# Kernel optimization log

Measured on AMD Instinct MI355X. Metric: run time of the kernel, lower is better.

## Reference

```python
import jax, jax.numpy as jnp
import numpy as np

B, S, F_IN = 2048, 256, 3
COND = 4
EMBED = 4
HID = 64
NUM_CODES = 256
BETA = 0.25


def _linear_params(key, fan_in, fan_out):
    k1, k2 = jax.random.split(key)
    lim = 1.0 / np.sqrt(fan_in)
    w = jax.random.uniform(k1, (fan_in, fan_out), jnp.float32, -lim, lim)
    b = jax.random.uniform(k2, (fan_out,), jnp.float32, -lim, lim)
    return w, b


def setup_inputs() -> dict:
    key = jax.random.key(0)
    ks = jax.random.split(key, 10)
    x = jax.random.normal(ks[0], (B, S, F_IN), jnp.float32)
    mask = jnp.ones((B, S), jnp.float32)
    x_conditional = jax.random.normal(ks[1], (B, COND), jnp.float32)
    enc_w1, enc_b1 = _linear_params(ks[2], F_IN + COND, HID)
    enc_w2, enc_b2 = _linear_params(ks[3], HID, HID)
    enc_w3, enc_b3 = _linear_params(ks[4], HID, EMBED)
    codebook = jax.random.normal(ks[5], (NUM_CODES, EMBED), jnp.float32)
    dec_w1, dec_b1 = _linear_params(ks[6], EMBED + COND, HID)
    dec_w2, dec_b2 = _linear_params(ks[7], HID, HID)
    dec_w3, dec_b3 = _linear_params(ks[8], HID, F_IN)
    return dict(x=x, mask=mask, x_conditional=x_conditional,
                enc_w1=enc_w1, enc_b1=enc_b1, enc_w2=enc_w2, enc_b2=enc_b2,
                enc_w3=enc_w3, enc_b3=enc_b3, codebook=codebook,
                dec_w1=dec_w1, dec_b1=dec_b1, dec_w2=dec_w2, dec_b2=dec_b2,
                dec_w3=dec_w3, dec_b3=dec_b3)


def _mlp(x, w1, b1, w2, b2, w3, b3):
    h = jax.nn.relu(x @ w1 + b1)
    h = jax.nn.relu(h @ w2 + b2)
    return h @ w3 + b3


def _vq(z, codebook):
    # z: [B, S, E]; nearest-codebook assignment via expanded squared L2
    zf = z.reshape(-1, z.shape[-1])                       # [N, E]
    d = (jnp.sum(zf * zf, axis=-1, keepdims=True)
         - 2.0 * zf @ codebook.T
         + jnp.sum(codebook * codebook, axis=-1))         # [N, num_codes]
    idx = jnp.argmin(d, axis=-1)                          # [N]
    z_q = codebook[idx].reshape(z.shape)                  # [B, S, E]
    # VQ losses (codebook + beta * commitment)
    loss = (jnp.mean((jax.lax.stop_gradient(z) - z_q) ** 2)
            + BETA * jnp.mean((z - jax.lax.stop_gradient(z_q)) ** 2))
    # straight-through estimator
    z_q_st = z + jax.lax.stop_gradient(z_q - z)
    return z_q_st, loss, idx.reshape(z.shape[:-1])


def reference(x, mask, x_conditional,
              enc_w1, enc_b1, enc_w2, enc_b2, enc_w3, enc_b3,
              codebook,
              dec_w1, dec_b1, dec_w2, dec_b2, dec_w3, dec_b3):
    cond = jnp.broadcast_to(x_conditional[:, None, :], (B, S, COND))
    xin = jnp.concatenate([x, cond], axis=-1) * mask[..., None]
    z = _mlp(xin, enc_w1, enc_b1, enc_w2, enc_b2, enc_w3, enc_b3)
    z_q, vq_loss, idx = _vq(z, codebook)
    zdec = jnp.concatenate([z_q, cond], axis=-1) * mask[..., None]
    x_reco = _mlp(zdec, dec_w1, dec_b1, dec_w2, dec_b2, dec_w3, dec_b3)
    return x_reco, vq_loss, idx
```

## Files before the change

kernel.cpp:

```cpp
#include <hip/hip_runtime.h>
#include <hip/hip_bf16.h>

#define BB   2048
#define SS   256
#define NTOK (BB*SS)
#define FIN  3
#define CND  4
#define EMB  4
#define HID  64
#define NC   256
#define TPB  256

#define OF_EW1 0
#define OF_EB1 448
#define OF_EW2 512
#define OF_EB2 4608
#define OF_EW3 4672
#define OF_EB3 4928
#define OF_CB  4944
#define OF_CC  5968
#define OF_DW1 6224
#define OF_DB1 6736
#define OF_DW2 6800
#define OF_DB2 10896
#define OF_DW3 10960
#define OF_DB3 11152
#define SMEM_F 11168

__global__ __launch_bounds__(TPB, 2) void vqvae_fused(
        const float* __restrict__ x, const float* __restrict__ mask,
        const float* __restrict__ cond,
        const float* __restrict__ ew1, const float* __restrict__ eb1,
        const float* __restrict__ ew2, const float* __restrict__ eb2,
        const float* __restrict__ ew3, const float* __restrict__ eb3,
        const float* __restrict__ cb,
        const float* __restrict__ dw1, const float* __restrict__ db1,
        const float* __restrict__ dw2, const float* __restrict__ db2,
        const float* __restrict__ dw3, const float* __restrict__ db3,
        float* __restrict__ out, float* __restrict__ loss_ws) {
    __shared__ float smem[SMEM_F];
    const int tid = threadIdx.x;

    for (int i = tid; i < (FIN+CND)*HID; i += TPB) smem[OF_EW1+i] = ew1[i];
    for (int i = tid; i < HID;           i += TPB) smem[OF_EB1+i] = eb1[i];
    for (int i = tid; i < HID*HID;       i += TPB) smem[OF_EW2+i] = ew2[i];
    for (int i = tid; i < HID;           i += TPB) smem[OF_EB2+i] = eb2[i];
    for (int i = tid; i < HID*EMB;       i += TPB) smem[OF_EW3+i] = ew3[i];
    for (int i = tid; i < EMB;           i += TPB) smem[OF_EB3+i] = eb3[i];
    for (int i = tid; i < NC*EMB;        i += TPB) smem[OF_CB +i] = cb[i];
    for (int i = tid; i < (EMB+CND)*HID; i += TPB) smem[OF_DW1+i] = dw1[i];
    for (int i = tid; i < HID;           i += TPB) smem[OF_DB1+i] = db1[i];
    for (int i = tid; i < HID*HID;       i += TPB) smem[OF_DW2+i] = dw2[i];
    for (int i = tid; i < HID;           i += TPB) smem[OF_DB2+i] = db2[i];
    for (int i = tid; i < HID*FIN;       i += TPB) smem[OF_DW3+i] = dw3[i];
    for (int i = tid; i < FIN;           i += TPB) smem[OF_DB3+i] = db3[i];
    {
        float c0 = cb[tid*EMB+0], c1 = cb[tid*EMB+1];
        float c2 = cb[tid*EMB+2], c3 = cb[tid*EMB+3];
        smem[OF_CC+tid] = ((c0*c0 + c1*c1) + c2*c2) + c3*c3;
    }
    __syncthreads();

    const int n0 = blockIdx.x * (2*TPB) + tid;
    const int n1 = n0 + TPB;
    const float m0 = mask[n0];
    const float m1 = mask[n1];
    const int bu0 = n0 >> 8;
    const int bu1 = bu0 + 1;

    float xin0[FIN+CND], xin1[FIN+CND];
    #pragma unroll
    for (int i = 0; i < FIN; i++) xin0[i] = x[n0*FIN + i] * m0;
    #pragma unroll
    for (int i = 0; i < FIN; i++) xin1[i] = x[n1*FIN + i] * m1;
    #pragma unroll
    for (int i = 0; i < CND; i++) xin0[FIN+i] = cond[bu0*CND + i] * m0;
    #pragma unroll
    for (int i = 0; i < CND; i++) xin1[FIN+i] = cond[bu1*CND + i] * m1;

    float hA[HID], hB[HID];
    #pragma unroll
    for (int j = 0; j < HID; j++) {
        float w0 = smem[OF_EW1 + j];
        float a = xin0[0] * w0;
        float b = xin1[0] * w0;
        #pragma unroll
        for (int i = 1; i < FIN+CND; i++) {
            float wi = smem[OF_EW1 + i*HID + j];
            a = fmaf(xin0[i], wi, a);
            b = fmaf(xin1[i], wi, b);
        }
        float bias = smem[OF_EB1 + j];
        hA[j] = fmaxf(a + bias, 0.0f);
        hB[j] = fmaxf(b + bias, 0.0f);
    }

    float z0 = 0.f, z1 = 0.f, z2 = 0.f, z3 = 0.f;
    float y0 = 0.f, y1 = 0.f, y2 = 0.f, y3 = 0.f;
    for (int jt = 0; jt < 16; jt++) {
        float a0 = 0.f, a1 = 0.f, a2 = 0.f, a3 = 0.f;
        float b0 = 0.f, b1 = 0.f, b2 = 0.f, b3 = 0.f;
        #pragma unroll
        for (int k = 0; k < HID; k++) {
            float4 w = *(const float4*)&smem[OF_EW2 + k*HID + jt*4];
            a0 = fmaf(hA[k], w.x, a0);
            a1 = fmaf(hA[k], w.y, a1);
            a2 = fmaf(hA[k], w.z, a2);
            a3 = fmaf(hA[k], w.w, a3);
            b0 = fmaf(hB[k], w.x, b0);
            b1 = fmaf(hB[k], w.y, b1);
            b2 = fmaf(hB[k], w.z, b2);
            b3 = fmaf(hB[k], w.w, b3);
        }
        float4 bb = *(const float4*)&smem[OF_EB2 + jt*4];
        float ta0 = fmaxf(a0 + bb.x, 0.0f), tb0 = fmaxf(b0 + bb.x, 0.0f);
        float ta1 = fmaxf(a1 + bb.y, 0.0f), tb1 = fmaxf(b1 + bb.y, 0.0f);
        float ta2 = fmaxf(a2 + bb.z, 0.0f), tb2 = fmaxf(b2 + bb.z, 0.0f);
        float ta3 = fmaxf(a3 + bb.w, 0.0f), tb3 = fmaxf(b3 + bb.w, 0.0f);
        float4 w0 = *(const float4*)&smem[OF_EW3 + (jt*4+0)*EMB];
        z0 = fmaf(ta0, w0.x, z0); z1 = fmaf(ta0, w0.y, z1);
        z2 = fmaf(ta0, w0.z, z2); z3 = fmaf(ta0, w0.w, z3);
        y0 = fmaf(tb0, w0.x, y0); y1 = fmaf(tb0, w0.y, y1);
        y2 = fmaf(tb0, w0.z, y2); y3 = fmaf(tb0, w0.w, y3);
        float4 w1 = *(const float4*)&smem[OF_EW3 + (jt*4+1)*EMB];
        z0 = fmaf(ta1, w1.x, z0); z1 = fmaf(ta1, w1.y, z1);
        z2 = fmaf(ta1, w1.z, z2); z3 = fmaf(ta1, w1.w, z3);
        y0 = fmaf(tb1, w1.x, y0); y1 = fmaf(tb1, w1.y, y1);
        y2 = fmaf(tb1, w1.z, y2); y3 = fmaf(tb1, w1.w, y3);
        float4 w2 = *(const float4*)&smem[OF_EW3 + (jt*4+2)*EMB];
        z0 = fmaf(ta2, w2.x, z0); z1 = fmaf(ta2, w2.y, z1);
        z2 = fmaf(ta2, w2.z, z2); z3 = fmaf(ta2, w2.w, z3);
        y0 = fmaf(tb2, w2.x, y0); y1 = fmaf(tb2, w2.y, y1);
        y2 = fmaf(tb2, w2.z, y2); y3 = fmaf(tb2, w2.w, y3);
        float4 w3 = *(const float4*)&smem[OF_EW3 + (jt*4+3)*EMB];
        z0 = fmaf(ta3, w3.x, z0); z1 = fmaf(ta3, w3.y, z1);
        z2 = fmaf(ta3, w3.z, z2); z3 = fmaf(ta3, w3.w, z3);
        y0 = fmaf(tb3, w3.x, y0); y1 = fmaf(tb3, w3.y, y1);
        y2 = fmaf(tb3, w3.z, y2); y3 = fmaf(tb3, w3.w, y3);
    }
    z0 += smem[OF_EB3+0]; z1 += smem[OF_EB3+1];
    z2 += smem[OF_EB3+2]; z3 += smem[OF_EB3+3];
    y0 += smem[OF_EB3+0]; y1 += smem[OF_EB3+1];
    y2 += smem[OF_EB3+2]; y3 += smem[OF_EB3+3];

    const float zzA = ((z0*z0 + z1*z1) + z2*z2) + z3*z3;
    const float zzB = ((y0*y0 + y1*y1) + y2*y2) + y3*y3;
    float bestA = 3.4e38f, bestB = 3.4e38f;
    int   biA = 0, biB = 0;
    #pragma unroll 4
    for (int ci = 0; ci < NC; ci++) {
        float4 c = *(const float4*)&smem[OF_CB + ci*EMB];
        float cc = smem[OF_CC + ci];
        float dotA = z0 * c.x;
        dotA = fmaf(z1, c.y, dotA);
        dotA = fmaf(z2, c.z, dotA);
        dotA = fmaf(z3, c.w, dotA);
        float dA = (zzA - 2.0f*dotA) + cc;
        if (dA < bestA) { bestA = dA; biA = ci; }
        float dotB = y0 * c.x;
        dotB = fmaf(y1, c.y, dotB);
        dotB = fmaf(y2, c.z, dotB);
        dotB = fmaf(y3, c.w, dotB);
        float dB = (zzB - 2.0f*dotB) + cc;
        if (dB < bestB) { bestB = dB; biB = ci; }
    }
    float4 qA = *(const float4*)&smem[OF_CB + biA*EMB];
    float4 qB = *(const float4*)&smem[OF_CB + biB*EMB];

    float e0 = z0-qA.x, e1 = z1-qA.y, e2 = z2-qA.z, e3 = z3-qA.w;
    float f0 = y0-qB.x, f1 = y1-qB.y, f2 = y2-qB.z, f3 = y3-qB.w;
    float sq = (((e0*e0 + e1*e1) + e2*e2) + e3*e3)
             + (((f0*f0 + f1*f1) + f2*f2) + f3*f3);
    #pragma unroll
    for (int off = 32; off > 0; off >>= 1) sq += __shfl_down(sq, off, 64);
    if ((tid & 63) == 0) atomicAdd(loss_ws, sq);

    out[NTOK*FIN + 1 + n0] = (float)biA;
    out[NTOK*FIN + 1 + n1] = (float)biB;

    float zd0[EMB+CND], zd1[EMB+CND];
    zd0[0] = qA.x*m0; zd0[1] = qA.y*m0; zd0[2] = qA.z*m0; zd0[3] = qA.w*m0;
    zd1[0] = qB.x*m1; zd1[1] = qB.y*m1; zd1[2] = qB.z*m1; zd1[3] = qB.w*m1;
    #pragma unroll
    for (int i = 0; i < CND; i++) zd0[EMB+i] = cond[bu0*CND + i] * m0;
    #pragma unroll
    for (int i = 0; i < CND; i++) zd1[EMB+i] = cond[bu1*CND + i] * m1;

    #pragma unroll
    for (int j = 0; j < HID; j++) {
        float w0 = smem[OF_DW1 + j];
        float a = zd0[0] * w0;
        float b = zd1[0] * w0;
        #pragma unroll
        for (int i = 1; i < EMB+CND; i++) {
            float wi = smem[OF_DW1 + i*HID + j];
            a = fmaf(zd0[i], wi, a);
            b = fmaf(zd1[i], wi, b);
        }
        float bias = smem[OF_DB1 + j];
        hA[j] = fmaxf(a + bias, 0.0f);
        hB[j] = fmaxf(b + bias, 0.0f);
    }

    float r0 = 0.f, r1 = 0.f, r2 = 0.f;
    float s0 = 0.f, s1 = 0.f, s2 = 0.f;
    for (int jt = 0; jt < 16; jt++) {
        float a0 = 0.f, a1 = 0.f, a2 = 0.f, a3 = 0.f;
        float b0 = 0.f, b1 = 0.f, b2 = 0.f, b3 = 0.f;
        #pragma unroll
        for (int k = 0; k < HID; k++) {
            float4 w = *(const float4*)&smem[OF_DW2 + k*HID + jt*4];
            a0 = fmaf(hA[k], w.x, a0);
            a1 = fmaf(hA[k], w.y, a1);
            a2 = fmaf(hA[k], w.z, a2);
            a3 = fmaf(hA[k], w.w, a3);
            b0 = fmaf(hB[k], w.x, b0);
            b1 = fmaf(hB[k], w.y, b1);
            b2 = fmaf(hB[k], w.z, b2);
            b3 = fmaf(hB[k], w.w, b3);
        }
        float4 bb = *(const float4*)&smem[OF_DB2 + jt*4];
        float ta0 = fmaxf(a0 + bb.x, 0.0f), tb0 = fmaxf(b0 + bb.x, 0.0f);
        float ta1 = fmaxf(a1 + bb.y, 0.0f), tb1 = fmaxf(b1 + bb.y, 0.0f);
        float ta2 = fmaxf(a2 + bb.z, 0.0f), tb2 = fmaxf(b2 + bb.z, 0.0f);
        float ta3 = fmaxf(a3 + bb.w, 0.0f), tb3 = fmaxf(b3 + bb.w, 0.0f);
        #pragma unroll
        for (int jj = 0; jj < 4; jj++) {
            float ta = (jj==0)?ta0:(jj==1)?ta1:(jj==2)?ta2:ta3;
            float tb = (jj==0)?tb0:(jj==1)?tb1:(jj==2)?tb2:tb3;
            int j = jt*4 + jj;
            float w0 = smem[OF_DW3 + j*FIN + 0];
            float w1 = smem[OF_DW3 + j*FIN + 1];
            float w2 = smem[OF_DW3 + j*FIN + 2];
            r0 = fmaf(ta, w0, r0); s0 = fmaf(tb, w0, s0);
            r1 = fmaf(ta, w1, r1); s1 = fmaf(tb, w1, s1);
            r2 = fmaf(ta, w2, r2); s2 = fmaf(tb, w2, s2);
        }
    }
    r0 += smem[OF_DB3+0]; r1 += smem[OF_DB3+1]; r2 += smem[OF_DB3+2];
    s0 += smem[OF_DB3+0]; s1 += smem[OF_DB3+1]; s2 += smem[OF_DB3+2];

    out[n0*FIN + 0] = r0;
    out[n0*FIN + 1] = r1;
    out[n0*FIN + 2] = r2;
    out[n1*FIN + 0] = s0;
    out[n1*FIN + 1] = s1;
    out[n1*FIN + 2] = s2;
}

__global__ void finalize_kernel(float* out, const float* loss_ws) {
    out[NTOK*FIN] = 1.25f * loss_ws[0] * (1.0f / (float)(NTOK*EMB));
}

extern "C" void kernel_launch(void* const* d_in, const int* in_sizes, int n_in,
                              void* d_out, int out_size, void* d_ws, size_t ws_size,
                              hipStream_t stream) {
    (void)in_sizes; (void)n_in; (void)ws_size; (void)out_size;
    float* ws = (float*)d_ws;
    hipMemsetAsync(ws, 0, sizeof(float), stream);

    vqvae_fused<<<NTOK/(2*TPB), TPB, 0, stream>>>(
        (const float*)d_in[0], (const float*)d_in[1], (const float*)d_in[2],
        (const float*)d_in[3], (const float*)d_in[4], (const float*)d_in[5],
        (const float*)d_in[6], (const float*)d_in[7], (const float*)d_in[8],
        (const float*)d_in[9], (const float*)d_in[10], (const float*)d_in[11],
        (const float*)d_in[12], (const float*)d_in[13], (const float*)d_in[14],
        (const float*)d_in[15],
        (float*)d_out, ws);

    finalize_kernel<<<1, 1, 0, stream>>>((float*)d_out, ws);
}
```

Baseline: 277.2 us.

## Read big weights and codebook from global via scalar/vector loads, transpose small layers in LDS

The 64x64 hidden weights and the codebook are no longer staged in shared memory. They are read directly from global memory through pointers offset by an opaque register zero, which steers the compiler toward vector-memory loads that are uniform across the wave and likely cache-served. The first-layer and last-layer weights are transposed and padded in LDS so each hidden unit takes two float4 reads, and the encoder bias is folded into the padding slot. This cuts LDS footprint and LDS read traffic, at the cost of relying on L1/L2 cache hits for the weight reads in the hot loops.

```diff
diff --git a/kernel.cpp b/kernel.cpp
--- a/kernel.cpp
+++ b/kernel.cpp
@@ -11,21 +11,17 @@
 #define NC   256
 #define TPB  256
 
-#define OF_EW1 0
-#define OF_EB1 448
-#define OF_EW2 512
-#define OF_EB2 4608
-#define OF_EW3 4672
-#define OF_EB3 4928
-#define OF_CB  4944
-#define OF_CC  5968
-#define OF_DW1 6224
-#define OF_DB1 6736
-#define OF_DW2 6800
-#define OF_DB2 10896
-#define OF_DW3 10960
-#define OF_DB3 11152
-#define SMEM_F 11168
+#define OF_EW1T 0
+#define OF_DW1T 512
+#define OF_DB1  1024
+#define OF_EB2  1088
+#define OF_DB2  1152
+#define OF_EW3  1216
+#define OF_EB3  1472
+#define OF_DB3  1476
+#define OF_DW3T 1480
+#define OF_CC   1736
+#define SMEM_F  1992
 
 __global__ __launch_bounds__(TPB, 2) void vqvae_fused(
         const float* __restrict__ x, const float* __restrict__ mask,
@@ -41,19 +37,33 @@
     __shared__ float smem[SMEM_F];
     const int tid = threadIdx.x;
 
-    for (int i = tid; i < (FIN+CND)*HID; i += TPB) smem[OF_EW1+i] = ew1[i];
-    for (int i = tid; i < HID;           i += TPB) smem[OF_EB1+i] = eb1[i];
-    for (int i = tid; i < HID*HID;       i += TPB) smem[OF_EW2+i] = ew2[i];
-    for (int i = tid; i < HID;           i += TPB) smem[OF_EB2+i] = eb2[i];
-    for (int i = tid; i < HID*EMB;       i += TPB) smem[OF_EW3+i] = ew3[i];
-    for (int i = tid; i < EMB;           i += TPB) smem[OF_EB3+i] = eb3[i];
-    for (int i = tid; i < NC*EMB;        i += TPB) smem[OF_CB +i] = cb[i];
-    for (int i = tid; i < (EMB+CND)*HID; i += TPB) smem[OF_DW1+i] = dw1[i];
-    for (int i = tid; i < HID;           i += TPB) smem[OF_DB1+i] = db1[i];
-    for (int i = tid; i < HID*HID;       i += TPB) smem[OF_DW2+i] = dw2[i];
-    for (int i = tid; i < HID;           i += TPB) smem[OF_DB2+i] = db2[i];
-    for (int i = tid; i < HID*FIN;       i += TPB) smem[OF_DW3+i] = dw3[i];
-    for (int i = tid; i < FIN;           i += TPB) smem[OF_DB3+i] = db3[i];
+    int vz = 0;
+    asm volatile("" : "+v"(vz));
+    const float* __restrict__ ew2v = ew2 + vz;
+    const float* __restrict__ dw2v = dw2 + vz;
+    const float* __restrict__ cbv  = cb  + vz;
+
+    for (int idx = tid; idx < (FIN+CND)*HID; idx += TPB) {
+        int i = idx >> 6, j = idx & 63;
+        smem[OF_EW1T + j*8 + i] = ew1[idx];
+    }
+    for (int j = tid; j < HID; j += TPB) smem[OF_EW1T + j*8 + 7] = eb1[j];
+    for (int idx = tid; idx < (EMB+CND)*HID; idx += TPB) {
+        int i = idx >> 6, j = idx & 63;
+        smem[OF_DW1T + j*8 + i] = dw1[idx];
+    }
+    for (int j = tid; j < HID; j += TPB) smem[OF_DB1 + j] = db1[j];
+    for (int j = tid; j < HID; j += TPB) smem[OF_EB2 + j] = eb2[j];
+    for (int j = tid; j < HID; j += TPB) smem[OF_DB2 + j] = db2[j];
+    for (int i = tid; i < HID*EMB; i += TPB) smem[OF_EW3 + i] = ew3[i];
+    for (int i = tid; i < EMB; i += TPB) smem[OF_EB3 + i] = eb3[i];
+    for (int i = tid; i < FIN; i += TPB) smem[OF_DB3 + i] = db3[i];
+    for (int j = tid; j < HID; j += TPB) {
+        smem[OF_DW3T + j*4 + 0] = dw3[j*FIN + 0];
+        smem[OF_DW3T + j*4 + 1] = dw3[j*FIN + 1];
+        smem[OF_DW3T + j*4 + 2] = dw3[j*FIN + 2];
+        smem[OF_DW3T + j*4 + 3] = 0.0f;
+    }
     {
         float c0 = cb[tid*EMB+0], c1 = cb[tid*EMB+1];
         float c2 = cb[tid*EMB+2], c3 = cb[tid*EMB+3];
@@ -81,18 +91,18 @@
     float hA[HID], hB[HID];
     #pragma unroll
     for (int j = 0; j < HID; j++) {
-        float w0 = smem[OF_EW1 + j];
-        float a = xin0[0] * w0;
-        float b = xin1[0] * w0;
-        #pragma unroll
-        for (int i = 1; i < FIN+CND; i++) {
-            float wi = smem[OF_EW1 + i*HID + j];
-            a = fmaf(xin0[i], wi, a);
-            b = fmaf(xin1[i], wi, b);
-        }
-        float bias = smem[OF_EB1 + j];
-        hA[j] = fmaxf(a + bias, 0.0f);
-        hB[j] = fmaxf(b + bias, 0.0f);
+        float4 lo = *(const float4*)&smem[OF_EW1T + j*8 + 0];
+        float4 hi = *(const float4*)&smem[OF_EW1T + j*8 + 4];
+        float a = xin0[0] * lo.x;
+        float b = xin1[0] * lo.x;
+        a = fmaf(xin0[1], lo.y, a);  b = fmaf(xin1[1], lo.y, b);
+        a = fmaf(xin0[2], lo.z, a);  b = fmaf(xin1[2], lo.z, b);
+        a = fmaf(xin0[3], lo.w, a);  b = fmaf(xin1[3], lo.w, b);
+        a = fmaf(xin0[4], hi.x, a);  b = fmaf(xin1[4], hi.x, b);
+        a = fmaf(xin0[5], hi.y, a);  b = fmaf(xin1[5], hi.y, b);
+        a = fmaf(xin0[6], hi.z, a);  b = fmaf(xin1[6], hi.z, b);
+        hA[j] = fmaxf(a + hi.w, 0.0f);
+        hB[j] = fmaxf(b + hi.w, 0.0f);
     }
 
     float z0 = 0.f, z1 = 0.f, z2 = 0.f, z3 = 0.f;
@@ -102,7 +112,7 @@
         float b0 = 0.f, b1 = 0.f, b2 = 0.f, b3 = 0.f;
         #pragma unroll
         for (int k = 0; k < HID; k++) {
-            float4 w = *(const float4*)&smem[OF_EW2 + k*HID + jt*4];
+            float4 w = *(const float4*)&ew2v[k*HID + jt*4];
             a0 = fmaf(hA[k], w.x, a0);
             a1 = fmaf(hA[k], w.y, a1);
             a2 = fmaf(hA[k], w.z, a2);
@@ -149,7 +159,7 @@
     int   biA = 0, biB = 0;
     #pragma unroll 4
     for (int ci = 0; ci < NC; ci++) {
-        float4 c = *(const float4*)&smem[OF_CB + ci*EMB];
+        float4 c = *(const float4*)&cbv[ci*EMB];
         float cc = smem[OF_CC + ci];
         float dotA = z0 * c.x;
         dotA = fmaf(z1, c.y, dotA);
@@ -164,8 +174,8 @@
         float dB = (zzB - 2.0f*dotB) + cc;
         if (dB < bestB) { bestB = dB; biB = ci; }
     }
-    float4 qA = *(const float4*)&smem[OF_CB + biA*EMB];
-    float4 qB = *(const float4*)&smem[OF_CB + biB*EMB];
+    float4 qA = *(const float4*)&cbv[biA*EMB];
+    float4 qB = *(const float4*)&cbv[biB*EMB];
 
     float e0 = z0-qA.x, e1 = z1-qA.y, e2 = z2-qA.z, e3 = z3-qA.w;
     float f0 = y0-qB.x, f1 = y1-qB.y, f2 = y2-qB.z, f3 = y3-qB.w;
@@ -188,15 +198,17 @@
 
     #pragma unroll
     for (int j = 0; j < HID; j++) {
-        float w0 = smem[OF_DW1 + j];
-        float a = zd0[0] * w0;
-        float b = zd1[0] * w0;
-        #pragma unroll
-        for (int i = 1; i < EMB+CND; i++) {
-            float wi = smem[OF_DW1 + i*HID + j];
-            a = fmaf(zd0[i], wi, a);
-            b = fmaf(zd1[i], wi, b);
-        }
+        float4 lo = *(const float4*)&smem[OF_DW1T + j*8 + 0];
+        float4 hi = *(const float4*)&smem[OF_DW1T + j*8 + 4];
+        float a = zd0[0] * lo.x;
+        float b = zd1[0] * lo.x;
+        a = fmaf(zd0[1], lo.y, a);  b = fmaf(zd1[1], lo.y, b);
+        a = fmaf(zd0[2], lo.z, a);  b = fmaf(zd1[2], lo.z, b);
+        a = fmaf(zd0[3], lo.w, a);  b = fmaf(zd1[3], lo.w, b);
+        a = fmaf(zd0[4], hi.x, a);  b = fmaf(zd1[4], hi.x, b);
+        a = fmaf(zd0[5], hi.y, a);  b = fmaf(zd1[5], hi.y, b);
+        a = fmaf(zd0[6], hi.z, a);  b = fmaf(zd1[6], hi.z, b);
+        a = fmaf(zd0[7], hi.w, a);  b = fmaf(zd1[7], hi.w, b);
         float bias = smem[OF_DB1 + j];
         hA[j] = fmaxf(a + bias, 0.0f);
         hB[j] = fmaxf(b + bias, 0.0f);
@@ -209,7 +221,7 @@
         float b0 = 0.f, b1 = 0.f, b2 = 0.f, b3 = 0.f;
         #pragma unroll
         for (int k = 0; k < HID; k++) {
-            float4 w = *(const float4*)&smem[OF_DW2 + k*HID + jt*4];
+            float4 w = *(const float4*)&dw2v[k*HID + jt*4];
             a0 = fmaf(hA[k], w.x, a0);
             a1 = fmaf(hA[k], w.y, a1);
             a2 = fmaf(hA[k], w.z, a2);
@@ -229,12 +241,10 @@
             float ta = (jj==0)?ta0:(jj==1)?ta1:(jj==2)?ta2:ta3;
             float tb = (jj==0)?tb0:(jj==1)?tb1:(jj==2)?tb2:tb3;
             int j = jt*4 + jj;
-            float w0 = smem[OF_DW3 + j*FIN + 0];
-            float w1 = smem[OF_DW3 + j*FIN + 1];
-            float w2 = smem[OF_DW3 + j*FIN + 2];
-            r0 = fmaf(ta, w0, r0); s0 = fmaf(tb, w0, s0);
-            r1 = fmaf(ta, w1, r1); s1 = fmaf(tb, w1, s1);
-            r2 = fmaf(ta, w2, r2); s2 = fmaf(tb, w2, s2);
+            float4 w = *(const float4*)&smem[OF_DW3T + j*4];
+            r0 = fmaf(ta, w.x, r0); s0 = fmaf(tb, w.x, s0);
+            r1 = fmaf(ta, w.y, r1); s1 = fmaf(tb, w.y, s1);
+            r2 = fmaf(ta, w.z, r2); s2 = fmaf(tb, w.z, s2);
         }
     }
     r0 += smem[OF_DB3+0]; r1 += smem[OF_DB3+1]; r2 += smem[OF_DB3+2];
```

Result: slower. 438.0 us (+58.0%).
